# Kernel tuning notes

Hardware: AMD Instinct MI355X
Metric: run time of the kernel (lower is better)

## Reference

```python
import jax, jax.numpy as jnp
import numpy as np

DIM = 512
HEADS = 8
DIM_KEY = 32          # dim_key * heads * 2 == DIM (required by the module's own einsum)
NUM_EXPERTS = 65536
NUM_KEYS = 256        # sqrt(NUM_EXPERTS)
TOPK = 16             # product_key_topk == num_experts_per_head
BN_EPS = 1e-5         # flax BatchNorm eps; running stats at init => x / sqrt(1 + eps)


def setup_inputs() -> dict:
    key = jax.random.key(0)
    k1, k2, k3, k4, k5 = jax.random.split(key, 5)
    b, n = 2, 512
    x = jax.random.normal(k1, (b, n, DIM), dtype=jnp.float32)
    # Dense(dim_key*heads*2, use_bias=False): lecun-normal-ish scale
    w_q = jax.random.normal(k2, (DIM, DIM_KEY * HEADS * 2), dtype=jnp.float32) / np.sqrt(DIM)
    # params created with nn.initializers.normal() -> stddev 0.01
    keys = jax.random.normal(k3, (HEADS, NUM_KEYS, 2, DIM_KEY), dtype=jnp.float32) * 0.01
    weight_down_embed = jax.random.normal(k4, (NUM_EXPERTS, DIM), dtype=jnp.float32) * 0.01
    weight_up_embed = jax.random.normal(k5, (NUM_EXPERTS, DIM), dtype=jnp.float32) * 0.01
    return {"x": x, "w_q": w_q, "keys": keys,
            "weight_down_embed": weight_down_embed, "weight_up_embed": weight_up_embed}


def peer_forward(x, w_q, keys, weight_down_embed, weight_up_embed):
    b, n, _ = x.shape
    # to_queries: Dense (no bias) -> BatchNorm in eval mode with init running stats
    # (mean=0, var=1, scale=1, bias=0) -> pure rescale; Dropout(0.0) is identity.
    q = (x @ w_q) * (1.0 / np.sqrt(1.0 + BN_EPS))            # [b, n, DIM]
    # rearrange b n (p h d) -> p b n h d  with p=2
    queries = q.reshape(b, n, 2, HEADS, DIM_KEY).transpose(2, 0, 1, 3, 4)
    sim = jnp.einsum('pbnhd,hkpd->pbnhk', queries, keys)     # [2, b, n, h, NUM_KEYS]
    v0, i0 = jax.lax.top_k(sim[0], TOPK)
    v1, i1 = jax.lax.top_k(sim[1], TOPK)
    # NOTE: faithful to the source's tuple unpacking, which assigns
    # scores_x=v0 (values), scores_y=i0 (indices of axis 0); v1/i1 feed the
    # (unused) all_indices path. So the combined score is values0 + indices0.
    all_scores = v0[..., :, None] + i0[..., None, :].astype(v0.dtype)  # [b,n,h,TOPK,TOPK]
    all_scores = all_scores.reshape(*all_scores.shape[:-2], -1)        # [b,n,h,TOPK*TOPK]
    scores, pk_indices = jax.lax.top_k(all_scores, TOPK)               # [b,n,h,TOPK]
    # Faithful to source: gathers use pk_indices (positions in the TOPK^2 list),
    # NOT the remapped expert ids (`indices` is computed but never used).
    weights_down = jnp.take(weight_down_embed, pk_indices, axis=0)     # [b,n,h,k,DIM]
    weights_up = jnp.take(weight_up_embed, pk_indices, axis=0)         # [b,n,h,k,DIM]
    h = jnp.einsum('bnd,bnhkd->bnhk', q, weights_down)
    h = jax.nn.gelu(h)                                                 # approximate gelu (flax default)
    h = h * jax.nn.softmax(scores, axis=-1)
    out = jnp.einsum('bnhk,bnhkd->bnd', h, weights_up)                 # [b, n, DIM]
    return out


def reference(x, w_q, keys, weight_down_embed, weight_up_embed):
    return peer_forward(x, w_q, keys, weight_down_embed, weight_up_embed)
```

## Files before the change

### kernel.cpp

```cpp
#include <hip/hip_runtime.h>
#include <math.h>

#define DIM    512
#define HEADS  8
#define DK     32
#define NKEYS  256
#define PKTOP  16
#define NTOK   1024

__device__ __forceinline__ float gelu_t(float x)
{
    float x3 = x * x * x;
    return 0.5f * x * (1.f + tanhf(0.7978845608028654f * (x + 0.044715f * x3)));
}

template<bool BT, int EPI, bool ZW>
__global__ __launch_bounds__(64)
void wgemm(const float* __restrict__ A, const float* __restrict__ B,
           float* __restrict__ C, int M, int N, int K, float scale,
           float* __restrict__ WS)
{
    __shared__ float As[64][36];
    __shared__ float Bs[64][36];
    const int lane = threadIdx.x;
    const int mg   = lane >> 3;
    const int ng   = lane & 7;
    const int m0   = blockIdx.y * 32;
    const int n0   = blockIdx.x * 32;

    if (ZW) {
        const int bid = blockIdx.y * gridDim.x + blockIdx.x;
        float4 z = make_float4(0.f, 0.f, 0.f, 0.f);
        *(float4*)(WS + (size_t)bid * 512 + lane * 8)     = z;
        *(float4*)(WS + (size_t)bid * 512 + lane * 8 + 4) = z;
    }

    const int r16 = lane >> 4;
    const int c16 = lane & 15;
    const int r8  = lane >> 3;
    const int c8  = lane & 7;

    float acc[4][4] = {{0.f}};

    for (int k0 = 0; k0 < K; k0 += 64) {
#pragma unroll
        for (int it = 0; it < 8; ++it) {
            int row  = r16 + 4 * it;
            float4 v = *(const float4*)(A + (size_t)(m0 + row) * K + k0 + c16 * 4);
            As[c16 * 4 + 0][row] = v.x; As[c16 * 4 + 1][row] = v.y;
            As[c16 * 4 + 2][row] = v.z; As[c16 * 4 + 3][row] = v.w;
        }
        if (!BT) {
#pragma unroll
            for (int it = 0; it < 8; ++it) {
                int kr   = r8 + 8 * it;
                float4 v = *(const float4*)(B + (size_t)(k0 + kr) * N + n0 + c8 * 4);
                *(float4*)&Bs[kr][c8 * 4] = v;
            }
        } else {
#pragma unroll
            for (int it = 0; it < 8; ++it) {
                int nr   = r16 + 4 * it;
                float4 v = *(const float4*)(B + (size_t)(n0 + nr) * K + k0 + c16 * 4);
                Bs[c16 * 4 + 0][nr] = v.x; Bs[c16 * 4 + 1][nr] = v.y;
                Bs[c16 * 4 + 2][nr] = v.z; Bs[c16 * 4 + 3][nr] = v.w;
            }
        }
        __syncthreads();
#pragma unroll
        for (int k = 0; k < 64; ++k) {
            float4 a = *(const float4*)&As[k][mg * 4];
            float4 b = *(const float4*)&Bs[k][ng * 4];
            float af[4] = {a.x, a.y, a.z, a.w};
            float bf[4] = {b.x, b.y, b.z, b.w};
#pragma unroll
            for (int i = 0; i < 4; ++i)
#pragma unroll
                for (int j = 0; j < 4; ++j) acc[i][j] += af[i] * bf[j];
        }
        __syncthreads();
    }

#pragma unroll
    for (int i = 0; i < 4; ++i) {
        int m = m0 + mg * 4 + i;
        float4 o;
        if (EPI == 1) {
            float4 w = *(const float4*)(WS + (size_t)m * N + n0 + ng * 4);
            o.x = gelu_t(acc[i][0]) * w.x;
            o.y = gelu_t(acc[i][1]) * w.y;
            o.z = gelu_t(acc[i][2]) * w.z;
            o.w = gelu_t(acc[i][3]) * w.w;
        } else {
            o = make_float4(acc[i][0] * scale, acc[i][1] * scale,
                            acc[i][2] * scale, acc[i][3] * scale);
        }
        *(float4*)(C + (size_t)m * N + n0 + ng * 4) = o;
    }
}

__global__ __launch_bounds__(256)
void k_simtopk(const float* __restrict__ q, const float* __restrict__ keys,
               float* __restrict__ wsum)
{
    const int lane = threadIdx.x & 63;
    const int th   = blockIdx.x * 4 + (threadIdx.x >> 6);
    const int t    = th >> 3;
    const int hh   = th & 7;
    const int base = lane * 4;

    const float4* qv = (const float4*)(q + (size_t)t * DIM + hh * DK);
    float4 qr[8];
#pragma unroll
    for (int i = 0; i < 8; ++i) qr[i] = qv[i];

    float v1[4];
#pragma unroll
    for (int j = 0; j < 4; ++j) {
        int k = base + j;
        const float4* kv = (const float4*)(keys + ((size_t)hh * NKEYS + k) * 2 * DK);
        float s = 0.f;
#pragma unroll
        for (int i = 0; i < 8; ++i) {
            float4 kk = kv[i];
            s += kk.x * qr[i].x + kk.y * qr[i].y + kk.z * qr[i].z + kk.w * qr[i].w;
        }
        v1[j] = s;
    }

    float my_v0 = 0.f;
    int   my_i0[4] = {0, 0, 0, 0};
#pragma unroll
    for (int r = 0; r < 16; ++r) {
        float b = v1[0]; int bj = 0;
        if (v1[1] > b) { b = v1[1]; bj = 1; }
        if (v1[2] > b) { b = v1[2]; bj = 2; }
        if (v1[3] > b) { b = v1[3]; bj = 3; }
        float m = b;
#pragma unroll
        for (int off = 32; off; off >>= 1) m = fmaxf(m, __shfl_xor(m, off, 64));
        unsigned long long bal = __ballot(b == m);
        int wl   = __ffsll((long long)bal) - 1;
        int widx = __shfl(base + bj, wl, 64);
        if ((lane >> 2) == r)       my_v0        = m;
        if ((lane & 3) == (r >> 2)) my_i0[r & 3] = widx;
        if (lane == wl) v1[bj] = -INFINITY;
    }

    float v2[4];
#pragma unroll
    for (int jj = 0; jj < 4; ++jj) v2[jj] = my_v0 + (float)my_i0[jj];

    float sc0 = 0.f, ssum = 0.f, my_sc = 0.f;
    int   my_pk = 0;
#pragma unroll
    for (int r = 0; r < 16; ++r) {
        float b = v2[0]; int bj = 0;
        if (v2[1] > b) { b = v2[1]; bj = 1; }
        if (v2[2] > b) { b = v2[2]; bj = 2; }
        if (v2[3] > b) { b = v2[3]; bj = 3; }
        float m = b;
#pragma unroll
        for (int off = 32; off; off >>= 1) m = fmaxf(m, __shfl_xor(m, off, 64));
        unsigned long long bal = __ballot(b == m);
        int wl = __ffsll((long long)bal) - 1;
        int wc = __shfl(base + bj, wl, 64);
        if (r == 0) sc0 = m;
        ssum += expf(m - sc0);
        if (lane == r) { my_sc = m; my_pk = wc; }
        if (lane == wl) v2[bj] = -INFINITY;
    }
    if (lane < PKTOP)
        atomicAdd(&wsum[(size_t)t * NKEYS + my_pk], expf(my_sc - sc0) / ssum);
}

extern "C" void kernel_launch(void* const* d_in, const int* in_sizes, int n_in,
                              void* d_out, int out_size, void* d_ws, size_t ws_size,
                              hipStream_t stream)
{
    const float* x    = (const float*)d_in[0];
    const float* wq   = (const float*)d_in[1];
    const float* keys = (const float*)d_in[2];
    const float* wd   = (const float*)d_in[3];
    const float* wu   = (const float*)d_in[4];
    float* out = (float*)d_out;

    float* q    = (float*)d_ws;
    float* Cb   = q + NTOK * DIM;
    float* wsum = Cb + NTOK * NKEYS;

    const float bnscale = 1.0f / sqrtf(1.0f + 1e-5f);

    wgemm<false, 0, true>
        <<<dim3(DIM / 32, NTOK / 32), 64, 0, stream>>>(x, wq, q, NTOK, DIM, DIM,
                                                       bnscale, wsum);

    k_simtopk<<<dim3(NTOK * HEADS / 4), 256, 0, stream>>>(q, keys, wsum);

    wgemm<true, 1, false>
        <<<dim3(NKEYS / 32, NTOK / 32), 64, 0, stream>>>(q, wd, Cb, NTOK, NKEYS,
                                                         DIM, 1.f, wsum);

    wgemm<false, 0, false>
        <<<dim3(DIM / 32, NTOK / 32), 64, 0, stream>>>(Cb, wu, out, NTOK, DIM,
                                                       NKEYS, 1.f, (float*)nullptr);
}
```

Before: 338.7 us.

## Split GEMM K-dimension across two waves with register prefetch and LDS reduction

Each 32x32 GEMM tile block now runs two wavefronts, each handling half of the K range in its own LDS buffers, and the partial sums are combined through a shared reduction buffer before the epilogue. Within each wave, the next K-chunk's global loads are issued into registers before the current chunk is computed, which removes the per-iteration block barriers. The goal is more in-flight waves and better latency hiding for these small-grid GEMMs. The cost is higher register use for the double-buffered float4 staging and extra LDS for the reduction.

```diff
diff --git a/kernel.cpp b/kernel.cpp
--- a/kernel.cpp
+++ b/kernel.cpp
@@ -14,15 +14,19 @@
     return 0.5f * x * (1.f + tanhf(0.7978845608028654f * (x + 0.044715f * x3)));
 }
 
-template<bool BT, int EPI, bool ZW>
-__global__ __launch_bounds__(64)
-void wgemm(const float* __restrict__ A, const float* __restrict__ B,
-           float* __restrict__ C, int M, int N, int K, float scale,
-           float* __restrict__ WS)
-{
-    __shared__ float As[64][36];
-    __shared__ float Bs[64][36];
-    const int lane = threadIdx.x;
+template<bool BT, int EPI, bool ZW, int T>
+__global__ __launch_bounds__(128)
+void wgemm2(const float* __restrict__ A, const float* __restrict__ B,
+            float* __restrict__ C, int M, int N, int K, float scale,
+            float* __restrict__ WS)
+{
+    __shared__ float As[2][64][36];
+    __shared__ float Bs[2][64][36];
+    __shared__ float red[32][36];
+
+    const int tid  = threadIdx.x;
+    const int w    = tid >> 6;
+    const int lane = tid & 63;
     const int mg   = lane >> 3;
     const int ng   = lane & 7;
     const int m0   = blockIdx.y * 32;
@@ -30,47 +34,63 @@
 
     if (ZW) {
         const int bid = blockIdx.y * gridDim.x + blockIdx.x;
-        float4 z = make_float4(0.f, 0.f, 0.f, 0.f);
-        *(float4*)(WS + (size_t)bid * 512 + lane * 8)     = z;
-        *(float4*)(WS + (size_t)bid * 512 + lane * 8 + 4) = z;
+        *(float4*)(WS + (size_t)bid * 512 + tid * 4) = make_float4(0.f, 0.f, 0.f, 0.f);
     }
 
     const int r16 = lane >> 4;
     const int c16 = lane & 15;
     const int r8  = lane >> 3;
     const int c8  = lane & 7;
+    const int kb0 = w * (T * 64);
+
+    auto loadAB = [&](float4 (&da)[8], float4 (&db)[8], int kbase) {
+#pragma unroll
+        for (int it = 0; it < 8; ++it)
+            da[it] = *(const float4*)(A + (size_t)(m0 + r16 + 4 * it) * K + kbase + c16 * 4);
+        if (!BT) {
+#pragma unroll
+            for (int it = 0; it < 8; ++it)
+                db[it] = *(const float4*)(B + (size_t)(kbase + r8 + 8 * it) * N + n0 + c8 * 4);
+        } else {
+#pragma unroll
+            for (int it = 0; it < 8; ++it)
+                db[it] = *(const float4*)(B + (size_t)(n0 + r16 + 4 * it) * K + kbase + c16 * 4);
+        }
+    };
+    auto storeAB = [&](const float4 (&da)[8], const float4 (&db)[8]) {
+#pragma unroll
+        for (int it = 0; it < 8; ++it) {
+            int row = r16 + 4 * it;
+            As[w][c16 * 4 + 0][row] = da[it].x; As[w][c16 * 4 + 1][row] = da[it].y;
+            As[w][c16 * 4 + 2][row] = da[it].z; As[w][c16 * 4 + 3][row] = da[it].w;
+        }
+        if (!BT) {
+#pragma unroll
+            for (int it = 0; it < 8; ++it)
+                *(float4*)&Bs[w][r8 + 8 * it][c8 * 4] = db[it];
+        } else {
+#pragma unroll
+            for (int it = 0; it < 8; ++it) {
+                int nr = r16 + 4 * it;
+                Bs[w][c16 * 4 + 0][nr] = db[it].x; Bs[w][c16 * 4 + 1][nr] = db[it].y;
+                Bs[w][c16 * 4 + 2][nr] = db[it].z; Bs[w][c16 * 4 + 3][nr] = db[it].w;
+            }
+        }
+    };
 
     float acc[4][4] = {{0.f}};
-
-    for (int k0 = 0; k0 < K; k0 += 64) {
-#pragma unroll
-        for (int it = 0; it < 8; ++it) {
-            int row  = r16 + 4 * it;
-            float4 v = *(const float4*)(A + (size_t)(m0 + row) * K + k0 + c16 * 4);
-            As[c16 * 4 + 0][row] = v.x; As[c16 * 4 + 1][row] = v.y;
-            As[c16 * 4 + 2][row] = v.z; As[c16 * 4 + 3][row] = v.w;
-        }
-        if (!BT) {
-#pragma unroll
-            for (int it = 0; it < 8; ++it) {
-                int kr   = r8 + 8 * it;
-                float4 v = *(const float4*)(B + (size_t)(k0 + kr) * N + n0 + c8 * 4);
-                *(float4*)&Bs[kr][c8 * 4] = v;
-            }
-        } else {
-#pragma unroll
-            for (int it = 0; it < 8; ++it) {
-                int nr   = r16 + 4 * it;
-                float4 v = *(const float4*)(B + (size_t)(n0 + nr) * K + k0 + c16 * 4);
-                Bs[c16 * 4 + 0][nr] = v.x; Bs[c16 * 4 + 1][nr] = v.y;
-                Bs[c16 * 4 + 2][nr] = v.z; Bs[c16 * 4 + 3][nr] = v.w;
-            }
-        }
-        __syncthreads();
+    float4 av[2][8], bv[2][8];
+
+    loadAB(av[0], bv[0], kb0);
+#pragma unroll
+    for (int t = 0; t < T; ++t) {
+        storeAB(av[t & 1], bv[t & 1]);
+        if (t + 1 < T)
+            loadAB(av[(t + 1) & 1], bv[(t + 1) & 1], kb0 + (t + 1) * 64);
 #pragma unroll
         for (int k = 0; k < 64; ++k) {
-            float4 a = *(const float4*)&As[k][mg * 4];
-            float4 b = *(const float4*)&Bs[k][ng * 4];
+            float4 a = *(const float4*)&As[w][k][mg * 4];
+            float4 b = *(const float4*)&Bs[w][k][ng * 4];
             float af[4] = {a.x, a.y, a.z, a.w};
             float bf[4] = {b.x, b.y, b.z, b.w};
 #pragma unroll
@@ -78,24 +98,32 @@
 #pragma unroll
                 for (int j = 0; j < 4; ++j) acc[i][j] += af[i] * bf[j];
         }
-        __syncthreads();
-    }
-
-#pragma unroll
-    for (int i = 0; i < 4; ++i) {
-        int m = m0 + mg * 4 + i;
-        float4 o;
-        if (EPI == 1) {
-            float4 w = *(const float4*)(WS + (size_t)m * N + n0 + ng * 4);
-            o.x = gelu_t(acc[i][0]) * w.x;
-            o.y = gelu_t(acc[i][1]) * w.y;
-            o.z = gelu_t(acc[i][2]) * w.z;
-            o.w = gelu_t(acc[i][3]) * w.w;
-        } else {
-            o = make_float4(acc[i][0] * scale, acc[i][1] * scale,
-                            acc[i][2] * scale, acc[i][3] * scale);
-        }
-        *(float4*)(C + (size_t)m * N + n0 + ng * 4) = o;
+    }
+
+    if (w == 1) {
+#pragma unroll
+        for (int i = 0; i < 4; ++i)
+            *(float4*)&red[mg * 4 + i][ng * 4] =
+                make_float4(acc[i][0], acc[i][1], acc[i][2], acc[i][3]);
+    }
+    __syncthreads();
+    if (w == 0) {
+#pragma unroll
+        for (int i = 0; i < 4; ++i) {
+            float4 r = *(const float4*)&red[mg * 4 + i][ng * 4];
+            float s0 = acc[i][0] + r.x, s1 = acc[i][1] + r.y;
+            float s2 = acc[i][2] + r.z, s3 = acc[i][3] + r.w;
+            int m = m0 + mg * 4 + i;
+            float4 o;
+            if (EPI == 1) {
+                float4 ww = *(const float4*)(WS + (size_t)m * N + n0 + ng * 4);
+                o.x = gelu_t(s0) * ww.x; o.y = gelu_t(s1) * ww.y;
+                o.z = gelu_t(s2) * ww.z; o.w = gelu_t(s3) * ww.w;
+            } else {
+                o = make_float4(s0 * scale, s1 * scale, s2 * scale, s3 * scale);
+            }
+            *(float4*)(C + (size_t)m * N + n0 + ng * 4) = o;
+        }
     }
 }
 
@@ -191,17 +219,17 @@
 
     const float bnscale = 1.0f / sqrtf(1.0f + 1e-5f);
 
-    wgemm<false, 0, true>
-        <<<dim3(DIM / 32, NTOK / 32), 64, 0, stream>>>(x, wq, q, NTOK, DIM, DIM,
-                                                       bnscale, wsum);
+    wgemm2<false, 0, true, 4>
+        <<<dim3(DIM / 32, NTOK / 32), 128, 0, stream>>>(x, wq, q, NTOK, DIM, DIM,
+                                                        bnscale, wsum);
 
     k_simtopk<<<dim3(NTOK * HEADS / 4), 256, 0, stream>>>(q, keys, wsum);
 
-    wgemm<true, 1, false>
-        <<<dim3(NKEYS / 32, NTOK / 32), 64, 0, stream>>>(q, wd, Cb, NTOK, NKEYS,
-                                                         DIM, 1.f, wsum);
-
-    wgemm<false, 0, false>
-        <<<dim3(DIM / 32, NTOK / 32), 64, 0, stream>>>(Cb, wu, out, NTOK, DIM,
-                                                       NKEYS, 1.f, (float*)nullptr);
-}
+    wgemm2<true, 1, false, 4>
+        <<<dim3(NKEYS / 32, NTOK / 32), 128, 0, stream>>>(q, wd, Cb, NTOK, NKEYS,
+                                                          DIM, 1.f, wsum);
+
+    wgemm2<false, 0, false, 2>
+        <<<dim3(DIM / 32, NTOK / 32), 128, 0, stream>>>(Cb, wu, out, NTOK, DIM,
+                                                        NKEYS, 1.f, (float*)nullptr);
+}
```

Measured after the change: 461.8 us. 36.3% more time.
